# Kernel tuning notes

Hardware: AMD Instinct MI355X
Metric: run time of the kernel (lower is better)

## Reference

```python
import jax, jax.numpy as jnp
import numpy as np

N_USERS = 100000
N_ITEMS = 200000
N = N_USERS + N_ITEMS
EMB_DIM = 64
NNZ = 9_600_000


def setup_inputs() -> dict:
    key = jax.random.key(0)
    ks = jax.random.split(key, 12)
    d = {
        'emb': jax.random.normal(ks[0], (N, EMB_DIM), jnp.float32) * 0.1,
        'gc_w0': jax.random.normal(ks[1], (64, 64), jnp.float32) * 0.1,
        'gc_b0': jax.random.normal(ks[2], (64,), jnp.float32) * 0.1,
        'bi_w0': jax.random.normal(ks[3], (64, 64), jnp.float32) * 0.1,
        'bi_b0': jax.random.normal(ks[4], (64,), jnp.float32) * 0.1,
        'gc_w1': jax.random.normal(ks[5], (64, 64), jnp.float32) * 0.1,
        'gc_b1': jax.random.normal(ks[6], (64,), jnp.float32) * 0.1,
        'bi_w1': jax.random.normal(ks[7], (64, 64), jnp.float32) * 0.1,
        'bi_b1': jax.random.normal(ks[8], (64,), jnp.float32) * 0.1,
        'adj_rows': jax.random.randint(ks[9], (NNZ,), 0, N, jnp.int32),
        'adj_cols': jax.random.randint(ks[10], (NNZ,), 0, N, jnp.int32),
        'adj_vals': jax.random.uniform(ks[11], (NNZ,), jnp.float32) * (1.0 / 32.0),
    }
    return d


def _ngcf_forward(emb, gc, bi, adj_rows, adj_cols, adj_vals):
    # gc, bi: lists of (W[out,in], b[out]) per layer
    ego = emb
    outs = [ego]
    for (gw, gb), (bw, bb) in zip(gc, bi):
        # sparse-dense matmul: side = A @ ego  (COO gather-multiply-scatter)
        side = jax.ops.segment_sum(adj_vals[:, None] * ego[adj_cols],
                                   adj_rows, num_segments=N)
        sum_e = (side + ego) @ gw.T + gb
        bi_e = (ego * side) @ bw.T + bb
        ego = jax.nn.leaky_relu(sum_e + bi_e, negative_slope=0.2)
        # F.dropout in eval mode is identity (training=False assumed)
        norm = ego / jnp.maximum(
            jnp.linalg.norm(ego, axis=1, keepdims=True), 1e-12)
        outs.append(norm)
    all_e = jnp.concatenate(outs, axis=1)  # [N, emb_dim * (1+L)]
    return all_e[:N_USERS], all_e[N_USERS:]


def reference(emb, gc_w0, gc_b0, bi_w0, bi_b0, gc_w1, gc_b1, bi_w1, bi_b1,
              adj_rows, adj_cols, adj_vals):
    gc = [(gc_w0, gc_b0), (gc_w1, gc_b1)]
    bi = [(bi_w0, bi_b0), (bi_w1, bi_b1)]
    return _ngcf_forward(emb, gc, bi, adj_rows, adj_cols, adj_vals)
```

## Files before the change

### kernel.cpp

```cpp
#include <hip/hip_runtime.h>
#include <hip/hip_bf16.h>

constexpr int N_NODES = 300000;
constexpr int DIM = 64;

constexpr int CHUNK  = 8192;
constexpr int B_ROWS = 256;
constexpr int NB_B   = (N_NODES + B_ROWS - 1) / B_ROWS;
constexpr int CAP    = 12288;
constexpr int SCAN_B = 4096;
constexpr int COL_MASK = (1 << 19) - 1;

typedef unsigned short ushort_t;
typedef unsigned char  uchar_t;
typedef __attribute__((ext_vector_type(8))) short bf16x8;
typedef __attribute__((ext_vector_type(4))) float f32x4;
typedef __attribute__((ext_vector_type(2))) float f32x2;

__device__ __forceinline__ float blo(unsigned u) { return __uint_as_float(u << 16); }
__device__ __forceinline__ float bhi(unsigned u) { return __uint_as_float(u & 0xffff0000u); }
__device__ __forceinline__ ushort_t f2b(float f) {
    unsigned u = __float_as_uint(f);
    return (ushort_t)((u + 0x7fffu + ((u >> 16) & 1u)) >> 16);
}

template<bool HI>
__device__ __forceinline__ f32x2 f8cvt2(unsigned u) {
#if __has_builtin(__builtin_amdgcn_cvt_pk_f32_fp8)
    return __builtin_amdgcn_cvt_pk_f32_fp8((int)u, HI);
#else
    unsigned b0 = (u >> (HI ? 16 : 0)) & 0xffu, b1 = (u >> (HI ? 24 : 8)) & 0xffu;
    f32x2 r;
    r[0] = __uint_as_float(((b0 & 0x80u) << 24) | ((b0 & 0x7fu) << 20)) * 0x1p120f;
    r[1] = __uint_as_float(((b1 & 0x80u) << 24) | ((b1 & 0x7fu) << 20)) * 0x1p120f;
    return r;
#endif
}

__device__ __forceinline__ unsigned sw_e4m3(float f) {
    unsigned u = __float_as_uint(f);
    unsigned s = (u >> 24) & 0x80u;
    float a = fabsf(f);
    if (a >= 464.f) return s | 0x7eu;
    int E = (int)((u >> 23) & 0xff) - 120;
    if (E >= 1) {
        unsigned m = u & 0x7fffffu;
        unsigned keep = m >> 20;
        unsigned rest = m & 0xfffffu;
        keep += (rest > 0x80000u || (rest == 0x80000u && (keep & 1u))) ? 1u : 0u;
        if (keep == 8u) { keep = 0u; E += 1; }
        if (E > 15 || (E == 15 && keep > 6u)) return s | 0x7eu;
        return s | ((unsigned)E << 3) | keep;
    } else {
        int q = (int)rintf(a * 512.f);
        if (q > 7) return s | 0x08u;
        return s | (unsigned)q;
    }
}

__device__ __forceinline__ unsigned f8pack4(float a, float b, float c, float d) {
#if __has_builtin(__builtin_amdgcn_cvt_pk_fp8_f32)
    int r = 0;
    r = __builtin_amdgcn_cvt_pk_fp8_f32(a, b, r, false);
    r = __builtin_amdgcn_cvt_pk_fp8_f32(c, d, r, true);
    return (unsigned)r;
#else
    return sw_e4m3(a) | (sw_e4m3(b) << 8) | (sw_e4m3(c) << 16) | (sw_e4m3(d) << 24);
#endif
}

__device__ __forceinline__ uchar_t f8pack1(float a) {
#if __has_builtin(__builtin_amdgcn_cvt_pk_fp8_f32)
    int r = __builtin_amdgcn_cvt_pk_fp8_f32(a, 0.f, 0, false);
    return (uchar_t)(r & 0xff);
#else
    return (uchar_t)sw_e4m3(a);
#endif
}

__global__ __launch_bounds__(256) void binhist_kernel(
    const int* __restrict__ rows, int* __restrict__ histT, int nnz)
{
    __shared__ int cnt[NB_B];
    for (int i = threadIdx.x; i < NB_B; i += 256) cnt[i] = 0;
    __syncthreads();
    int base = blockIdx.x * CHUNK;
#pragma unroll
    for (int k = 0; k < CHUNK / 256; ++k) {
        int e = base + k * 256 + threadIdx.x;
        if (e < nnz) atomicAdd(&cnt[rows[e] >> 8], 1);
    }
    __syncthreads();
    for (int b = threadIdx.x; b < NB_B; b += 256)
        histT[(size_t)blockIdx.x * NB_B + b] = cnt[b];
}

__global__ __launch_bounds__(256) void transpose_kernel(
    const int* __restrict__ in, int* __restrict__ out, int R, int C)
{
    __shared__ int tile[32][33];
    int c0 = blockIdx.x * 32, r0 = blockIdx.y * 32;
    int tx = threadIdx.x & 31, ty = threadIdx.x >> 5;
#pragma unroll
    for (int k = 0; k < 4; ++k) {
        int r = r0 + ty + k * 8, c = c0 + tx;
        if (r < R && c < C) tile[ty + k * 8][tx] = in[(size_t)r * C + c];
    }
    __syncthreads();
#pragma unroll
    for (int k = 0; k < 4; ++k) {
        int c = c0 + ty + k * 8, r = r0 + tx;
        if (c < C && r < R) out[(size_t)c * R + r] = tile[tx][ty + k * 8];
    }
}

__global__ __launch_bounds__(256) void scan1_kernel(
    int* __restrict__ a, int* __restrict__ bsum, int n)
{
    __shared__ int tsum[256];
    int base = blockIdx.x * SCAN_B;
    int v[16];
    int s = 0;
#pragma unroll
    for (int k = 0; k < 16; ++k) {
        int i = base + threadIdx.x * 16 + k;
        v[k] = (i < n) ? a[i] : 0;
        s += v[k];
    }
    tsum[threadIdx.x] = s;
    __syncthreads();
    for (int off = 1; off < 256; off <<= 1) {
        int u = (threadIdx.x >= off) ? tsum[threadIdx.x - off] : 0;
        __syncthreads();
        tsum[threadIdx.x] += u;
        __syncthreads();
    }
    int excl = (threadIdx.x == 0) ? 0 : tsum[threadIdx.x - 1];
#pragma unroll
    for (int k = 0; k < 16; ++k) {
        int i = base + threadIdx.x * 16 + k;
        if (i < n) a[i] = excl;
        excl += v[k];
    }
    if (threadIdx.x == 255) bsum[blockIdx.x] = tsum[255];
}

__global__ __launch_bounds__(256) void scan2_kernel(int* bsum, int nb)
{
    __shared__ int tsum[256];
    int v[8];
    int s = 0;
#pragma unroll
    for (int k = 0; k < 8; ++k) {
        int i = threadIdx.x * 8 + k;
        v[k] = (i < nb) ? bsum[i] : 0;
        s += v[k];
    }
    tsum[threadIdx.x] = s;
    __syncthreads();
    for (int off = 1; off < 256; off <<= 1) {
        int u = (threadIdx.x >= off) ? tsum[threadIdx.x - off] : 0;
        __syncthreads();
        tsum[threadIdx.x] += u;
        __syncthreads();
    }
    int excl = (threadIdx.x == 0) ? 0 : tsum[threadIdx.x - 1];
#pragma unroll
    for (int k = 0; k < 8; ++k) {
        int i = threadIdx.x * 8 + k;
        if (i < nb) bsum[i] = excl;
        excl += v[k];
    }
}

__global__ __launch_bounds__(256) void scan3_kernel(
    int* __restrict__ a, const int* __restrict__ bsum, int n)
{
    int i = blockIdx.x * 256 + threadIdx.x;
    if (i < n) a[i] += bsum[i >> 12];
}

__global__ __launch_bounds__(512) void binscatter_kernel(
    const int* __restrict__ rows, const int* __restrict__ cols,
    const float* __restrict__ vals, const int* __restrict__ curT,
    int2* __restrict__ meta, int nnz)
{
    __shared__ int2 cv[CHUNK];
    __shared__ int  dst[CHUNK];
    __shared__ int  cnt[NB_B];
    __shared__ int  loc[NB_B];
    __shared__ int  gb[NB_B];
    __shared__ int  tsum[512];

    const int tid  = threadIdx.x;
    const int base = blockIdx.x * CHUNK;

    for (int b = tid; b < NB_B; b += 512) cnt[b] = 0;
    __syncthreads();

    int rb[16], pk[16], vb[16];
#pragma unroll
    for (int k = 0; k < 16; ++k) {
        int e = base + k * 512 + tid;
        if (e < nnz) {
            int r = rows[e];
            rb[k] = r >> 8;
            pk[k] = cols[e] | ((r & 255) << 19);
            vb[k] = __float_as_int(vals[e]);
            atomicAdd(&cnt[rb[k]], 1);
        } else rb[k] = -1;
    }
    __syncthreads();

    int i0 = tid * 3;
    int c0 = 0, c1 = 0, c2 = 0, s = 0;
    if (i0     < NB_B) { c0 = cnt[i0];     s += c0; }
    if (i0 + 1 < NB_B) { c1 = cnt[i0 + 1]; s += c1; }
    if (i0 + 2 < NB_B) { c2 = cnt[i0 + 2]; s += c2; }
    tsum[tid] = s;
    __syncthreads();
    for (int off = 1; off < 512; off <<= 1) {
        int u = (tid >= off) ? tsum[tid - off] : 0;
        __syncthreads();
        tsum[tid] += u;
        __syncthreads();
    }
    int ex = (tid == 0) ? 0 : tsum[tid - 1];
    if (i0     < NB_B) { loc[i0]     = ex; ex += c0; }
    if (i0 + 1 < NB_B) { loc[i0 + 1] = ex; ex += c1; }
    if (i0 + 2 < NB_B) { loc[i0 + 2] = ex; ex += c2; }
    __syncthreads();

    for (int b = tid; b < NB_B; b += 512) {
        gb[b]  = curT[(size_t)blockIdx.x * NB_B + b];
        cnt[b] = 0;
    }
    __syncthreads();

#pragma unroll
    for (int k = 0; k < 16; ++k) {
        if (rb[k] >= 0) {
            int b   = rb[k];
            int off = atomicAdd(&cnt[b], 1);
            int p   = loc[b] + off;
            cv[p]   = make_int2(pk[k], vb[k]);
            dst[p]  = gb[b] + off;
        }
    }
    __syncthreads();

    int n = min(nnz - base, CHUNK);
    for (int i = tid; i < n; i += 512)
        meta[dst[i]] = cv[i];
}

__global__ __launch_bounds__(256) void bucketfinal_kernel(
    const int* __restrict__ histS,
    int2* __restrict__ meta,
    int* __restrict__ row_ptr, int nnz, int nch)
{
    __shared__ int2 cv[CAP];
    __shared__ int cnt[256], scn[256], cur[256];

    int b    = blockIdx.x;
    int base = histS[(size_t)b * nch];
    int end  = (b + 1 < gridDim.x) ? histS[(size_t)(b + 1) * nch] : nnz;
    int n    = min(end - base, CAP);

    cnt[threadIdx.x] = 0;
    __syncthreads();
    for (int i = threadIdx.x; i < n; i += 256) {
        int2 m = meta[base + i];
        cv[i] = m;
        atomicAdd(&cnt[(m.x >> 19) & 255], 1);
    }
    __syncthreads();
    int v = cnt[threadIdx.x];
    scn[threadIdx.x] = v;
    __syncthreads();
    for (int off = 1; off < 256; off <<= 1) {
        int u = (threadIdx.x >= off) ? scn[threadIdx.x - off] : 0;
        __syncthreads();
        scn[threadIdx.x] += u;
        __syncthreads();
    }
    int excl = scn[threadIdx.x] - v;

    int r0 = b * B_ROWS;
    int nr = min(B_ROWS, N_NODES - r0);
    if (threadIdx.x < nr) row_ptr[r0 + threadIdx.x] = base + excl;
    if (b == gridDim.x - 1 && threadIdx.x == 0) row_ptr[N_NODES] = nnz;

    cur[threadIdx.x] = excl;
    __syncthreads();
    for (int i = threadIdx.x; i < n; i += 256) {
        int2 m = cv[i];
        int d = atomicAdd(&cur[(m.x >> 19) & 255], 1);
        meta[base + d] = m;
    }
}

__global__ __launch_bounds__(256) void emb_prep_kernel(
    const float4* __restrict__ emb, unsigned* __restrict__ tblF8,
    float4* __restrict__ out)
{
    int i = blockIdx.x * 256 + threadIdx.x;
    if (i >= N_NODES * 16) return;
    float4 x = emb[i];
    int n = i >> 4, j = i & 15;
    out[(size_t)n * 48 + j] = x;
    tblF8[i] = f8pack4(x.x, x.y, x.z, x.w);
}

__global__ __launch_bounds__(256) void spmm_csr_f8_kernel(
    const uint2* __restrict__ tbl8,
    const int*   __restrict__ row_ptr,
    const int2*  __restrict__ meta,
    float*       __restrict__ side)
{
    int wid = (blockIdx.x * 256 + threadIdx.x) >> 6;
    if (wid >= N_NODES) return;
    int lane = threadIdx.x & 63;
    int g = lane >> 3;
    int q = lane & 7;

    int start = row_ptr[wid];
    int end   = row_ptr[wid + 1];

    float acc[8];
#pragma unroll
    for (int i = 0; i < 8; ++i) acc[i] = 0.f;

    for (int j = start + g; j < end; j += 8) {
        int2 m = meta[j];
        float v = __int_as_float(m.y);
        uint2 x = tbl8[(size_t)(m.x & COL_MASK) * 8 + q];
        f32x2 f0 = f8cvt2<false>(x.x), f1 = f8cvt2<true>(x.x);
        f32x2 f2 = f8cvt2<false>(x.y), f3 = f8cvt2<true>(x.y);
        acc[0] += v * f0[0]; acc[1] += v * f0[1];
        acc[2] += v * f1[0]; acc[3] += v * f1[1];
        acc[4] += v * f2[0]; acc[5] += v * f2[1];
        acc[6] += v * f3[0]; acc[7] += v * f3[1];
    }
#pragma unroll
    for (int off = 8; off <= 32; off <<= 1) {
#pragma unroll
        for (int i = 0; i < 8; ++i) acc[i] += __shfl_xor(acc[i], off);
    }
    if (g == 0) {
        float4* dst = (float4*)(side + (size_t)wid * DIM + q * 8);
        dst[0] = make_float4(acc[0], acc[1], acc[2], acc[3]);
        dst[1] = make_float4(acc[4], acc[5], acc[6], acc[7]);
    }
}

template<bool EGO_F32, bool WRITE_TBL>
__global__ __launch_bounds__(256) void dense_mfma_kernel(
    const float*   __restrict__ ego_f32,
    const ushort_t* __restrict__ ego_b16,
    const float* __restrict__ side,
    const float* __restrict__ gw, const float* __restrict__ gb,
    const float* __restrict__ bw, const float* __restrict__ bb,
    ushort_t* __restrict__ tblb_out,
    uchar_t*  __restrict__ tblf8_out,
    float* __restrict__ out, int out_col)
{
    __shared__ ushort_t s_lds[64][72];
    __shared__ ushort_t p_lds[64][72];

    const int tid  = threadIdx.x;
    const int lane = tid & 63;
    const int wv   = tid >> 6;
    const int lrow = lane & 15;
    const int kgrp = lane >> 4;

    bf16x8 wgf[4][2], wbf[4][2];
    float  biasv[4];
#pragma unroll
    for (int t = 0; t < 4; ++t) {
        int o = 16 * t + lrow;
#pragma unroll
        for (int h = 0; h < 2; ++h) {
            const float* pg = gw + (size_t)o * DIM + 32 * h + 8 * kgrp;
            const float* pb = bw + (size_t)o * DIM + 32 * h + 8 * kgrp;
            ushort_t tg[8], tb[8];
#pragma unroll
            for (int i = 0; i < 8; ++i) { tg[i] = f2b(pg[i]); tb[i] = f2b(pb[i]); }
            wgf[t][h] = *(const bf16x8*)tg;
            wbf[t][h] = *(const bf16x8*)tb;
        }
        biasv[t] = gb[o] + bb[o];
    }

    for (int tile0 = blockIdx.x * 64; tile0 < N_NODES; tile0 += gridDim.x * 64) {
        int nmax = min(64, N_NODES - tile0);
        __syncthreads();
        {
            int r  = tid >> 2;
            int d0 = (tid & 3) * 16;
            if (r < nmax) {
                const float4* sp = (const float4*)(side + (size_t)(tile0 + r) * DIM + d0);
                float4 s0 = sp[0], s1 = sp[1], s2 = sp[2], s3 = sp[3];
                float sv[16] = { s0.x, s0.y, s0.z, s0.w, s1.x, s1.y, s1.z, s1.w,
                                 s2.x, s2.y, s2.z, s2.w, s3.x, s3.y, s3.z, s3.w };
                float ev[16];
                if (EGO_F32) {
                    const float4* ep = (const float4*)(ego_f32 + (size_t)(tile0 + r) * DIM + d0);
                    float4 e0 = ep[0], e1 = ep[1], e2 = ep[2], e3 = ep[3];
                    float tmp[16] = { e0.x, e0.y, e0.z, e0.w, e1.x, e1.y, e1.z, e1.w,
                                      e2.x, e2.y, e2.z, e2.w, e3.x, e3.y, e3.z, e3.w };
#pragma unroll
                    for (int i = 0; i < 16; ++i) ev[i] = tmp[i];
                } else {
                    const uint4* ep = (const uint4*)(ego_b16 + (size_t)(tile0 + r) * DIM + d0);
                    uint4 e0 = ep[0], e1 = ep[1];
                    float tmp[16] = { blo(e0.x), bhi(e0.x), blo(e0.y), bhi(e0.y),
                                      blo(e0.z), bhi(e0.z), blo(e0.w), bhi(e0.w),
                                      blo(e1.x), bhi(e1.x), blo(e1.y), bhi(e1.y),
                                      blo(e1.z), bhi(e1.z), blo(e1.w), bhi(e1.w) };
#pragma unroll
                    for (int i = 0; i < 16; ++i) ev[i] = tmp[i];
                }
                unsigned spk[8], ppk[8];
#pragma unroll
                for (int i = 0; i < 8; ++i) {
                    float a  = sv[2*i]   + ev[2*i];
                    float b2 = sv[2*i+1] + ev[2*i+1];
                    float c  = sv[2*i]   * ev[2*i];
                    float d  = sv[2*i+1] * ev[2*i+1];
                    spk[i] = ((unsigned)f2b(b2) << 16) | f2b(a);
                    ppk[i] = ((unsigned)f2b(d)  << 16) | f2b(c);
                }
                *(uint4*)&s_lds[r][d0]     = make_uint4(spk[0], spk[1], spk[2], spk[3]);
                *(uint4*)&s_lds[r][d0 + 8] = make_uint4(spk[4], spk[5], spk[6], spk[7]);
                *(uint4*)&p_lds[r][d0]     = make_uint4(ppk[0], ppk[1], ppk[2], ppk[3]);
                *(uint4*)&p_lds[r][d0 + 8] = make_uint4(ppk[4], ppk[5], ppk[6], ppk[7]);
            }
        }
        __syncthreads();

        const int arow = wv * 16 + lrow;
        bf16x8 sf[2], pf[2];
        sf[0] = *(const bf16x8*)&s_lds[arow][8 * kgrp];
        sf[1] = *(const bf16x8*)&s_lds[arow][32 + 8 * kgrp];
        pf[0] = *(const bf16x8*)&p_lds[arow][8 * kgrp];
        pf[1] = *(const bf16x8*)&p_lds[arow][32 + 8 * kgrp];

        f32x4 acc[4];
#pragma unroll
        for (int t = 0; t < 4; ++t)
            acc[t] = (f32x4){biasv[t], biasv[t], biasv[t], biasv[t]};

#pragma unroll
        for (int h = 0; h < 2; ++h) {
#pragma unroll
            for (int t = 0; t < 4; ++t) {
                acc[t] = __builtin_amdgcn_mfma_f32_16x16x32_bf16(sf[h], wgf[t][h], acc[t], 0, 0, 0);
                acc[t] = __builtin_amdgcn_mfma_f32_16x16x32_bf16(pf[h], wbf[t][h], acc[t], 0, 0, 0);
            }
        }

        float y[4][4];
        float ssr[4] = {0.f, 0.f, 0.f, 0.f};
#pragma unroll
        for (int t = 0; t < 4; ++t)
#pragma unroll
            for (int rg = 0; rg < 4; ++rg) {
                float v = acc[t][rg];
                v = v > 0.f ? v : 0.2f * v;
                y[t][rg] = v;
                ssr[rg] += v * v;
            }
#pragma unroll
        for (int off = 1; off <= 8; off <<= 1)
#pragma unroll
            for (int rg = 0; rg < 4; ++rg)
                ssr[rg] += __shfl_xor(ssr[rg], off);

#pragma unroll
        for (int rg = 0; rg < 4; ++rg) {
            int node = tile0 + wv * 16 + kgrp * 4 + rg;
            if (node < N_NODES) {
                float inv = 1.0f / fmaxf(sqrtf(ssr[rg]), 1e-12f);
                float* orow = out + (size_t)node * 192 + out_col;
#pragma unroll
                for (int t = 0; t < 4; ++t)
                    orow[t * 16 + lrow] = y[t][rg] * inv;
                if (WRITE_TBL) {
#pragma unroll
                    for (int t = 0; t < 4; ++t) {
                        tblb_out[(size_t)node * DIM + t * 16 + lrow] = f2b(y[t][rg]);
                        tblf8_out[(size_t)node * DIM + t * 16 + lrow] = f8pack1(y[t][rg]);
                    }
                }
            }
        }
    }
}

__global__ __launch_bounds__(256) void spmm_atomic_kernel(
    const float* __restrict__ ego,
    const int*   __restrict__ rows,
    const int*   __restrict__ cols,
    const float* __restrict__ vals,
    float*       __restrict__ side,
    int nnz)
{
    long long i = (long long)blockIdx.x * blockDim.x + threadIdx.x;
    long long total = (long long)nnz * DIM;
    if (i >= total) return;
    int e = (int)(i >> 6);
    int d = (int)(i & 63);
    atomicAdd(side + ((size_t)rows[e] * DIM + d), vals[e] * ego[(size_t)cols[e] * DIM + d]);
}

template<bool WRITE_F32>
__global__ __launch_bounds__(256) void dense_norm_kernel(
    const float* __restrict__ ego_in,
    const float* __restrict__ side,
    const float* __restrict__ gw, const float* __restrict__ gb,
    const float* __restrict__ bw, const float* __restrict__ bb,
    float* __restrict__ ego_out,
    float* __restrict__ out, int out_col)
{
    __shared__ float s_lds[32][DIM];
    __shared__ float p_lds[32][DIM];

    const int o  = threadIdx.x & 63;
    const int wv = threadIdx.x >> 6;

    float w0[DIM], w1[DIM];
#pragma unroll
    for (int k4 = 0; k4 < DIM / 4; ++k4) {
        float4 a = *(const float4*)(gw + (size_t)o * DIM + k4 * 4);
        float4 b = *(const float4*)(bw + (size_t)o * DIM + k4 * 4);
        w0[4*k4+0] = a.x; w0[4*k4+1] = a.y; w0[4*k4+2] = a.z; w0[4*k4+3] = a.w;
        w1[4*k4+0] = b.x; w1[4*k4+1] = b.y; w1[4*k4+2] = b.z; w1[4*k4+3] = b.w;
    }
    const float bias = gb[o] + bb[o];

    for (int tile = blockIdx.x * 32; tile < N_NODES; tile += gridDim.x * 32) {
        int nmax = min(32, N_NODES - tile);
        __syncthreads();
        const float4* sd4 = (const float4*)side + (size_t)tile * 16;
        const float4* eg4 = (const float4*)ego_in + (size_t)tile * 16;
        float4* s4 = (float4*)&s_lds[0][0];
        float4* p4 = (float4*)&p_lds[0][0];
        for (int i = threadIdx.x; i < nmax * 16; i += 256) {
            float4 e = eg4[i], s = sd4[i];
            s4[i] = make_float4(s.x+e.x, s.y+e.y, s.z+e.z, s.w+e.w);
            p4[i] = make_float4(s.x*e.x, s.y*e.y, s.z*e.z, s.w*e.w);
        }
        __syncthreads();
        for (int n = wv; n < nmax; n += 4) {
            const float4* srow = (const float4*)&s_lds[n][0];
            const float4* prow = (const float4*)&p_lds[n][0];
            float a0 = bias, a1 = 0.f, a2 = 0.f, a3 = 0.f;
#pragma unroll
            for (int k4 = 0; k4 < 16; ++k4) {
                float4 sk = srow[k4];
                float4 pk = prow[k4];
                a0 = fmaf(sk.x, w0[4*k4+0], a0); a1 = fmaf(pk.x, w1[4*k4+0], a1);
                a2 = fmaf(sk.y, w0[4*k4+1], a2); a3 = fmaf(pk.y, w1[4*k4+1], a3);
                a0 = fmaf(sk.z, w0[4*k4+2], a0); a1 = fmaf(pk.z, w1[4*k4+2], a1);
                a2 = fmaf(sk.w, w0[4*k4+3], a2); a3 = fmaf(pk.w, w1[4*k4+3], a3);
            }
            float acc = (a0 + a1) + (a2 + a3);
            float y = acc > 0.f ? acc : 0.2f * acc;
            size_t node = (size_t)(tile + n);
            if (WRITE_F32) ego_out[node * DIM + o] = y;
            float ss = y * y;
#pragma unroll
            for (int off = 32; off > 0; off >>= 1)
                ss += __shfl_xor(ss, off);
            float inv = 1.0f / fmaxf(sqrtf(ss), 1e-12f);
            out[node * 192 + out_col + o] = y * inv;
        }
    }
}

__global__ __launch_bounds__(256) void copy_emb_kernel(
    const float4* __restrict__ emb, float4* __restrict__ out)
{
    int i = blockIdx.x * blockDim.x + threadIdx.x;
    if (i >= N_NODES * 16) return;
    int n = i >> 4, j = i & 15;
    out[(size_t)n * 48 + j] = emb[i];
}

extern "C" void kernel_launch(void* const* d_in, const int* in_sizes, int n_in,
                              void* d_out, int out_size, void* d_ws, size_t ws_size,
                              hipStream_t stream)
{
    const float* emb   = (const float*)d_in[0];
    const float* gc_w0 = (const float*)d_in[1];
    const float* gc_b0 = (const float*)d_in[2];
    const float* bi_w0 = (const float*)d_in[3];
    const float* bi_b0 = (const float*)d_in[4];
    const float* gc_w1 = (const float*)d_in[5];
    const float* gc_b1 = (const float*)d_in[6];
    const float* bi_w1 = (const float*)d_in[7];
    const float* bi_b1 = (const float*)d_in[8];
    const int*   rows  = (const int*)d_in[9];
    const int*   cols  = (const int*)d_in[10];
    const float* vals  = (const float*)d_in[11];
    const int    nnz   = in_sizes[9];

    float* out = (float*)d_out;

    const int nch = (nnz + CHUNK - 1) / CHUNK;
    const int n2  = NB_B * nch;
    const size_t hist_al = (((size_t)n2 * sizeof(int)) + 63) & ~size_t(63);
    const size_t tbl_al  = (((size_t)N_NODES * DIM) + 63) & ~size_t(63);

    char* ws = (char*)d_ws;
    size_t off = 0;
    auto alloc = [&](size_t bytes) { char* p = ws + off; off += (bytes + 63) & ~size_t(63); return p; };
    float* side = (float*)alloc((size_t)N_NODES * DIM * sizeof(float));
    ushort_t* ego1_b = (ushort_t*)alloc((size_t)N_NODES * DIM * sizeof(ushort_t));
    int2* meta = (int2*)alloc((size_t)nnz * sizeof(int2));
    size_t u_build = 2 * hist_al;
    char* U = alloc(u_build > tbl_al ? u_build : tbl_al);
    int* histT = (int*)U;
    int* histA = (int*)(U + hist_al);
    int* curT  = histT;
    uchar_t* emb_f8  = (uchar_t*)U;
    uchar_t* ego1_f8 = (uchar_t*)U;
    int* row_ptr = (int*)alloc((size_t)(N_NODES + 1) * sizeof(int));
    int* bsum    = (int*)alloc(2048 * sizeof(int));
    const bool csr_ok = (off <= ws_size) && (nnz <= 11000000);

    const int spmm_blocks  = (N_NODES * 64 + 255) / 256;
    const int dense_blocks = (N_NODES + 63) / 64;

    if (csr_ok) {
        binhist_kernel<<<nch, 256, 0, stream>>>(rows, histT, nnz);
        {
            dim3 g((NB_B + 31) / 32, (nch + 31) / 32);
            transpose_kernel<<<g, 256, 0, stream>>>(histT, histA, nch, NB_B);
        }
        const int nsb = (n2 + SCAN_B - 1) / SCAN_B;
        scan1_kernel<<<nsb, 256, 0, stream>>>(histA, bsum, n2);
        scan2_kernel<<<1, 256, 0, stream>>>(bsum, nsb);
        scan3_kernel<<<(n2 + 255) / 256, 256, 0, stream>>>(histA, bsum, n2);
        {
            dim3 g((nch + 31) / 32, (NB_B + 31) / 32);
            transpose_kernel<<<g, 256, 0, stream>>>(histA, curT, NB_B, nch);
        }
        binscatter_kernel<<<nch, 512, 0, stream>>>(rows, cols, vals, curT, meta, nnz);
        bucketfinal_kernel<<<NB_B, 256, 0, stream>>>(histA, meta, row_ptr, nnz, nch);

        emb_prep_kernel<<<(N_NODES * 16 + 255) / 256, 256, 0, stream>>>(
            (const float4*)emb, (unsigned*)emb_f8, (float4*)out);

        spmm_csr_f8_kernel<<<spmm_blocks, 256, 0, stream>>>(
            (const uint2*)emb_f8, row_ptr, meta, side);
        dense_mfma_kernel<true, true><<<dense_blocks, 256, 0, stream>>>(
            emb, nullptr, side, gc_w0, gc_b0, bi_w0, bi_b0,
            ego1_b, ego1_f8, out, DIM);

        spmm_csr_f8_kernel<<<spmm_blocks, 256, 0, stream>>>(
            (const uint2*)ego1_f8, row_ptr, meta, side);
        dense_mfma_kernel<false, false><<<dense_blocks, 256, 0, stream>>>(
            nullptr, ego1_b, side, gc_w1, gc_b1, bi_w1, bi_b1,
            nullptr, nullptr, out, 2 * DIM);
    } else {
        float* ego1 = (float*)meta;
        const size_t side_bytes = (size_t)N_NODES * DIM * sizeof(float);
        const long long total = (long long)nnz * DIM;
        const int ab = (int)((total + 255) / 256);
        const int db = (N_NODES + 31) / 32;
        hipMemsetAsync(side, 0, side_bytes, stream);
        spmm_atomic_kernel<<<ab, 256, 0, stream>>>(emb, rows, cols, vals, side, nnz);
        dense_norm_kernel<true><<<db, 256, 0, stream>>>(
            emb, side, gc_w0, gc_b0, bi_w0, bi_b0, ego1, out, DIM);
        hipMemsetAsync(side, 0, side_bytes, stream);
        spmm_atomic_kernel<<<ab, 256, 0, stream>>>(ego1, rows, cols, vals, side, nnz);
        dense_norm_kernel<false><<<db, 256, 0, stream>>>(
            ego1, side, gc_w1, gc_b1, bi_w1, bi_b1, nullptr, out, 2 * DIM);
        copy_emb_kernel<<<(N_NODES * 16 + 255) / 256, 256, 0, stream>>>(
            (const float4*)emb, (float4*)out);
    }
}
```

Baseline: 859.3 us.

## Compress CSR metadata to 4 bytes with fp8 values and store side in bf16

The final bucket pass now packs each edge into one 32-bit word: a 19-bit column index plus an fp8 value scaled by 512. The SpMM reads these 4-byte entries instead of 8-byte int2 and writes the side result as bf16 with non-temporal stores. The dense kernel then reads bf16 side, and the embedding copy to the output also uses non-temporal stores. Together this roughly halves metadata and side-buffer traffic, at the cost of extra precision loss from quantizing edge weights to fp8 and the side result to bf16.

```diff
diff --git a/kernel.cpp b/kernel.cpp
--- a/kernel.cpp
+++ b/kernel.cpp
@@ -10,12 +10,15 @@
 constexpr int CAP    = 12288;
 constexpr int SCAN_B = 4096;
 constexpr int COL_MASK = (1 << 19) - 1;
+constexpr float VAL_SCALE = 512.f;
+constexpr float VAL_INV   = 1.f / 512.f;
 
 typedef unsigned short ushort_t;
 typedef unsigned char  uchar_t;
 typedef __attribute__((ext_vector_type(8))) short bf16x8;
 typedef __attribute__((ext_vector_type(4))) float f32x4;
 typedef __attribute__((ext_vector_type(2))) float f32x2;
+typedef __attribute__((ext_vector_type(4))) unsigned u32x4;
 
 __device__ __forceinline__ float blo(unsigned u) { return __uint_as_float(u << 16); }
 __device__ __forceinline__ float bhi(unsigned u) { return __uint_as_float(u & 0xffff0000u); }
@@ -69,12 +72,12 @@
 #endif
 }
 
-__device__ __forceinline__ uchar_t f8pack1(float a) {
+__device__ __forceinline__ unsigned f8pack1(float a) {
 #if __has_builtin(__builtin_amdgcn_cvt_pk_fp8_f32)
     int r = __builtin_amdgcn_cvt_pk_fp8_f32(a, 0.f, 0, false);
-    return (uchar_t)(r & 0xff);
+    return (unsigned)(r & 0xff);
 #else
-    return (uchar_t)sw_e4m3(a);
+    return sw_e4m3(a);
 #endif
 }
 
@@ -256,10 +259,12 @@
 
 __global__ __launch_bounds__(256) void bucketfinal_kernel(
     const int* __restrict__ histS,
-    int2* __restrict__ meta,
+    const int2* __restrict__ meta,
+    unsigned* __restrict__ metaC,
     int* __restrict__ row_ptr, int nnz, int nch)
 {
-    __shared__ int2 cv[CAP];
+    __shared__ unsigned cc[CAP];
+    __shared__ uchar_t  lr[CAP];
     __shared__ int cnt[256], scn[256], cur[256];
 
     int b    = blockIdx.x;
@@ -271,8 +276,11 @@
     __syncthreads();
     for (int i = threadIdx.x; i < n; i += 256) {
         int2 m = meta[base + i];
-        cv[i] = m;
-        atomicAdd(&cnt[(m.x >> 19) & 255], 1);
+        int l = (m.x >> 19) & 255;
+        unsigned v8 = f8pack1(__int_as_float(m.y) * VAL_SCALE);
+        cc[i] = (unsigned)(m.x & COL_MASK) | (v8 << 19);
+        lr[i] = (uchar_t)l;
+        atomicAdd(&cnt[l], 1);
     }
     __syncthreads();
     int v = cnt[threadIdx.x];
@@ -294,29 +302,29 @@
     cur[threadIdx.x] = excl;
     __syncthreads();
     for (int i = threadIdx.x; i < n; i += 256) {
-        int2 m = cv[i];
-        int d = atomicAdd(&cur[(m.x >> 19) & 255], 1);
-        meta[base + d] = m;
+        int d = atomicAdd(&cur[lr[i]], 1);
+        metaC[base + d] = cc[i];
     }
 }
 
 __global__ __launch_bounds__(256) void emb_prep_kernel(
     const float4* __restrict__ emb, unsigned* __restrict__ tblF8,
-    float4* __restrict__ out)
+    float* __restrict__ out)
 {
     int i = blockIdx.x * 256 + threadIdx.x;
     if (i >= N_NODES * 16) return;
     float4 x = emb[i];
     int n = i >> 4, j = i & 15;
-    out[(size_t)n * 48 + j] = x;
+    f32x4 xv = {x.x, x.y, x.z, x.w};
+    __builtin_nontemporal_store(xv, (f32x4*)(out + (size_t)n * 192 + j * 4));
     tblF8[i] = f8pack4(x.x, x.y, x.z, x.w);
 }
 
 __global__ __launch_bounds__(256) void spmm_csr_f8_kernel(
     const uint2* __restrict__ tbl8,
     const int*   __restrict__ row_ptr,
-    const int2*  __restrict__ meta,
-    float*       __restrict__ side)
+    const unsigned* __restrict__ metaC,
+    ushort_t*    __restrict__ side_b16)
 {
     int wid = (blockIdx.x * 256 + threadIdx.x) >> 6;
     if (wid >= N_NODES) return;
@@ -332,9 +340,9 @@
     for (int i = 0; i < 8; ++i) acc[i] = 0.f;
 
     for (int j = start + g; j < end; j += 8) {
-        int2 m = meta[j];
-        float v = __int_as_float(m.y);
-        uint2 x = tbl8[(size_t)(m.x & COL_MASK) * 8 + q];
+        unsigned mc = metaC[j];
+        float v = f8cvt2<false>(mc >> 19)[0];
+        uint2 x = tbl8[(size_t)(mc & COL_MASK) * 8 + q];
         f32x2 f0 = f8cvt2<false>(x.x), f1 = f8cvt2<true>(x.x);
         f32x2 f2 = f8cvt2<false>(x.y), f3 = f8cvt2<true>(x.y);
         acc[0] += v * f0[0]; acc[1] += v * f0[1];
@@ -348,9 +356,12 @@
         for (int i = 0; i < 8; ++i) acc[i] += __shfl_xor(acc[i], off);
     }
     if (g == 0) {
-        float4* dst = (float4*)(side + (size_t)wid * DIM + q * 8);
-        dst[0] = make_float4(acc[0], acc[1], acc[2], acc[3]);
-        dst[1] = make_float4(acc[4], acc[5], acc[6], acc[7]);
+        u32x4 pk;
+        pk.x = ((unsigned)f2b(acc[1] * VAL_INV) << 16) | f2b(acc[0] * VAL_INV);
+        pk.y = ((unsigned)f2b(acc[3] * VAL_INV) << 16) | f2b(acc[2] * VAL_INV);
+        pk.z = ((unsigned)f2b(acc[5] * VAL_INV) << 16) | f2b(acc[4] * VAL_INV);
+        pk.w = ((unsigned)f2b(acc[7] * VAL_INV) << 16) | f2b(acc[6] * VAL_INV);
+        __builtin_nontemporal_store(pk, (u32x4*)(side_b16 + (size_t)wid * DIM + q * 8));
     }
 }
 
@@ -358,7 +369,7 @@
 __global__ __launch_bounds__(256) void dense_mfma_kernel(
     const float*   __restrict__ ego_f32,
     const ushort_t* __restrict__ ego_b16,
-    const float* __restrict__ side,
+    const ushort_t* __restrict__ side_b16,
     const float* __restrict__ gw, const float* __restrict__ gb,
     const float* __restrict__ bw, const float* __restrict__ bb,
     ushort_t* __restrict__ tblb_out,
@@ -399,10 +410,12 @@
             int r  = tid >> 2;
             int d0 = (tid & 3) * 16;
             if (r < nmax) {
-                const float4* sp = (const float4*)(side + (size_t)(tile0 + r) * DIM + d0);
-                float4 s0 = sp[0], s1 = sp[1], s2 = sp[2], s3 = sp[3];
-                float sv[16] = { s0.x, s0.y, s0.z, s0.w, s1.x, s1.y, s1.z, s1.w,
-                                 s2.x, s2.y, s2.z, s2.w, s3.x, s3.y, s3.z, s3.w };
+                const uint4* sp = (const uint4*)(side_b16 + (size_t)(tile0 + r) * DIM + d0);
+                uint4 sb0 = sp[0], sb1 = sp[1];
+                float sv[16] = { blo(sb0.x), bhi(sb0.x), blo(sb0.y), bhi(sb0.y),
+                                 blo(sb0.z), bhi(sb0.z), blo(sb0.w), bhi(sb0.w),
+                                 blo(sb1.x), bhi(sb1.x), blo(sb1.y), bhi(sb1.y),
+                                 blo(sb1.z), bhi(sb1.z), blo(sb1.w), bhi(sb1.w) };
                 float ev[16];
                 if (EGO_F32) {
                     const float4* ep = (const float4*)(ego_f32 + (size_t)(tile0 + r) * DIM + d0);
@@ -490,7 +503,7 @@
 #pragma unroll
                     for (int t = 0; t < 4; ++t) {
                         tblb_out[(size_t)node * DIM + t * 16 + lrow] = f2b(y[t][rg]);
-                        tblf8_out[(size_t)node * DIM + t * 16 + lrow] = f8pack1(y[t][rg]);
+                        tblf8_out[(size_t)node * DIM + t * 16 + lrow] = (uchar_t)f8pack1(y[t][rg]);
                     }
                 }
             }
@@ -616,7 +629,10 @@
     char* ws = (char*)d_ws;
     size_t off = 0;
     auto alloc = [&](size_t bytes) { char* p = ws + off; off += (bytes + 63) & ~size_t(63); return p; };
-    float* side = (float*)alloc((size_t)N_NODES * DIM * sizeof(float));
+    char* sideRegion = alloc((size_t)N_NODES * DIM * sizeof(float));
+    float*    side_f32 = (float*)sideRegion;
+    ushort_t* side_b16 = (ushort_t*)sideRegion;
+    unsigned* metaC    = (unsigned*)(sideRegion + (size_t)N_NODES * DIM * sizeof(ushort_t));
     ushort_t* ego1_b = (ushort_t*)alloc((size_t)N_NODES * DIM * sizeof(ushort_t));
     int2* meta = (int2*)alloc((size_t)nnz * sizeof(int2));
     size_t u_build = 2 * hist_al;
@@ -628,7 +644,8 @@
     uchar_t* ego1_f8 = (uchar_t*)U;
     int* row_ptr = (int*)alloc((size_t)(N_NODES + 1) * sizeof(int));
     int* bsum    = (int*)alloc(2048 * sizeof(int));
-    const bool csr_ok = (off <= ws_size) && (nnz <= 11000000);
+    const bool csr_ok = (off <= ws_size) && (nnz <= 11000000) &&
+                        ((size_t)nnz * 4 <= (size_t)N_NODES * DIM * 2);
 
     const int spmm_blocks  = (N_NODES * 64 + 255) / 256;
     const int dense_blocks = (N_NODES + 63) / 64;
@@ -648,21 +665,21 @@
             transpose_kernel<<<g, 256, 0, stream>>>(histA, curT, NB_B, nch);
         }
         binscatter_kernel<<<nch, 512, 0, stream>>>(rows, cols, vals, curT, meta, nnz);
-        bucketfinal_kernel<<<NB_B, 256, 0, stream>>>(histA, meta, row_ptr, nnz, nch);
+        bucketfinal_kernel<<<NB_B, 256, 0, stream>>>(histA, meta, metaC, row_ptr, nnz, nch);
 
         emb_prep_kernel<<<(N_NODES * 16 + 255) / 256, 256, 0, stream>>>(
-            (const float4*)emb, (unsigned*)emb_f8, (float4*)out);
+            (const float4*)emb, (unsigned*)emb_f8, out);
 
         spmm_csr_f8_kernel<<<spmm_blocks, 256, 0, stream>>>(
-            (const uint2*)emb_f8, row_ptr, meta, side);
+            (const uint2*)emb_f8, row_ptr, metaC, side_b16);
         dense_mfma_kernel<true, true><<<dense_blocks, 256, 0, stream>>>(
-            emb, nullptr, side, gc_w0, gc_b0, bi_w0, bi_b0,
+            emb, nullptr, side_b16, gc_w0, gc_b0, bi_w0, bi_b0,
             ego1_b, ego1_f8, out, DIM);
 
         spmm_csr_f8_kernel<<<spmm_blocks, 256, 0, stream>>>(
-            (const uint2*)ego1_f8, row_ptr, meta, side);
+            (const uint2*)ego1_f8, row_ptr, metaC, side_b16);
         dense_mfma_kernel<false, false><<<dense_blocks, 256, 0, stream>>>(
-            nullptr, ego1_b, side, gc_w1, gc_b1, bi_w1, bi_b1,
+            nullptr, ego1_b, side_b16, gc_w1, gc_b1, bi_w1, bi_b1,
             nullptr, nullptr, out, 2 * DIM);
     } else {
         float* ego1 = (float*)meta;
@@ -670,14 +687,14 @@
         const long long total = (long long)nnz * DIM;
         const int ab = (int)((total + 255) / 256);
         const int db = (N_NODES + 31) / 32;
-        hipMemsetAsync(side, 0, side_bytes, stream);
-        spmm_atomic_kernel<<<ab, 256, 0, stream>>>(emb, rows, cols, vals, side, nnz);
+        hipMemsetAsync(side_f32, 0, side_bytes, stream);
+        spmm_atomic_kernel<<<ab, 256, 0, stream>>>(emb, rows, cols, vals, side_f32, nnz);
         dense_norm_kernel<true><<<db, 256, 0, stream>>>(
-            emb, side, gc_w0, gc_b0, bi_w0, bi_b0, ego1, out, DIM);
-        hipMemsetAsync(side, 0, side_bytes, stream);
-        spmm_atomic_kernel<<<ab, 256, 0, stream>>>(ego1, rows, cols, vals, side, nnz);
+            emb, side_f32, gc_w0, gc_b0, bi_w0, bi_b0, ego1, out, DIM);
+        hipMemsetAsync(side_f32, 0, side_bytes, stream);
+        spmm_atomic_kernel<<<ab, 256, 0, stream>>>(ego1, rows, cols, vals, side_f32, nnz);
         dense_norm_kernel<false><<<db, 256, 0, stream>>>(
-            ego1, side, gc_w1, gc_b1, bi_w1, bi_b1, nullptr, out, 2 * DIM);
+            ego1, side_f32, gc_w1, gc_b1, bi_w1, bi_b1, nullptr, out, 2 * DIM);
         copy_emb_kernel<<<(N_NODES * 16 + 255) / 256, 256, 0, stream>>>(
             (const float4*)emb, (float4*)out);
     }
```

Measured after the change: 798.3 us. -7.1%, faster.
